# Kernel tuning notes

Measured on AMD Instinct MI355X. Metric: run time of the kernel, lower is better.

Reference implementation:

```python
import math
import jax, jax.numpy as jnp
import numpy as np

HEADS = 8
DIM_HEAD = 64
MAX_POS_EMB = 512


def setup_inputs() -> dict:
    key = jax.random.key(0)
    ks = jax.random.split(key, 6)
    dim = 512
    inner = HEADS * DIM_HEAD  # 512
    x = jax.random.normal(ks[0], (16, 3900, dim), jnp.float32)
    wq = jax.random.normal(ks[1], (dim, inner), jnp.float32) * 0.02
    wkv = jax.random.normal(ks[2], (dim, 2 * inner), jnp.float32) * 0.02
    wout_w = jax.random.normal(ks[3], (inner, dim), jnp.float32) * 0.02
    wout_b = jax.random.normal(ks[4], (dim,), jnp.float32) * 0.02
    rel_pos_table = jax.random.normal(ks[5], (2 * MAX_POS_EMB + 1, DIM_HEAD), jnp.float32) * 0.02
    return {"x": x, "wq": wq, "wkv": wkv, "wout_w": wout_w, "wout_b": wout_b,
            "rel_pos_table": rel_pos_table, "context_size": 200}


def reference(x, wq, wkv, wout_w, wout_b, rel_pos_table, context_size):
    bs, n, d = x.shape
    h, dh = HEADS, DIM_HEAD
    c = context_size
    scale = dh ** -0.5
    nb = math.ceil(n / c)
    nr = n % c
    if nr > 0:
        x = jnp.pad(x, ((0, 0), (0, c - nr), (0, 0)))  # [bs, nb*c, d]
    np_tok = nb * c
    q = x @ wq                     # [bs, np, inner]
    kv = x @ wkv                   # [bs, np, 2*inner]
    k, v = jnp.split(kv, 2, axis=-1)
    # [bs, nb, c, h, dh] -> [bs, nb, h, c, dh]
    def to_heads(t):
        return t.reshape(bs, nb, c, h, dh).transpose(0, 1, 3, 2, 4)
    q, k, v = to_heads(q), to_heads(k), to_heads(v)
    dots = jnp.einsum('bmhid,bmhjd->bmhij', q, k) * scale  # [bs, nb, h, c, c]
    # relative position bias (Transformer-XL style within chunk)
    seq = jnp.arange(c)
    dist = jnp.clip(seq[:, None] - seq[None, :], -c, c) + MAX_POS_EMB  # [c, c]
    rel = rel_pos_table[dist]  # [c, c, dh]
    pos_attn = jnp.einsum('bmhcd,crd->bmhcr', q, rel) * scale
    dots = dots + pos_attn
    if nr > 0:
        # last chunk: mask everything except the valid top-left nr x nr block
        mask = jnp.ones((c, c), dtype=bool).at[:nr, :nr].set(False)
        mask_value = -jnp.finfo(dots.dtype).max
        dots = dots.at[:, -1].set(jnp.where(mask, mask_value, dots[:, -1]))
    attn = jax.nn.softmax(dots, axis=-1)
    out = jnp.einsum('bmhij,bmhjd->bmhid', attn, v)  # [bs, nb, h, c, dh]
    out = out.transpose(0, 1, 3, 2, 4).reshape(bs, np_tok, h * dh)
    out = out[:, :n, :] @ wout_w + wout_b  # dropout is identity at eval
    return out
```

## Files before the change

### kernel.cpp

```cpp
#include <hip/hip_runtime.h>
#include <hip/hip_bf16.h>
#include <cstdint>
#include <cstddef>

#define BS 16
#define SEQ 3900
#define DIM 512
#define NHEAD 8
#define DH 64
#define CHUNK 200
#define NB 20
#define NR 100
#define NP 4000
#define MAXPOS 512
#define MD 62400

typedef __attribute__((ext_vector_type(8))) short bf16x8;
typedef __attribute__((ext_vector_type(8))) unsigned short u16x8;
typedef __attribute__((ext_vector_type(4))) float f32x4;
#define MFMA_BF16 __builtin_amdgcn_mfma_f32_16x16x32_bf16

static __device__ __forceinline__ float bf2f(unsigned short u) {
  union { unsigned int i; float f; } v; v.i = ((unsigned int)u) << 16; return v.f;
}
static __device__ __forceinline__ unsigned short f2bf(float f) {
  unsigned int x = __float_as_uint(f);
  unsigned int lsb = (x >> 16) & 1u;
  x += 0x7fffu + lsb;
  return (unsigned short)(x >> 16);
}

static __device__ __forceinline__ void gload16(const void* g, void* l) {
  auto gp = reinterpret_cast<const __attribute__((address_space(1))) unsigned int*>(
      reinterpret_cast<uintptr_t>(g));
  auto lp = reinterpret_cast<__attribute__((address_space(3))) unsigned int*>(
      reinterpret_cast<uintptr_t>(l));
  __builtin_amdgcn_global_load_lds(gp, lp, 16, 0, 0);
}

static __device__ __forceinline__ const unsigned short* wt_row(
    const unsigned short* base, int n) {
  unsigned ch = (unsigned)n / 100u;
  unsigned rr = (unsigned)n - ch * 100u;
  return base + (size_t)ch * (NP * DIM) + (size_t)SEQ * DIM + (size_t)rr * DIM;
}

__global__ __launch_bounds__(256) void prep_table(
    const float* __restrict__ table, unsigned short* __restrict__ Tb)
{
  int idx = (blockIdx.x * 256 + threadIdx.x) * 4;
  if (idx < 416 * 64) {
    float4 f = *reinterpret_cast<const float4*>(table + (size_t)305 * 64 + idx);
    ushort4 o;
    o.x = f2bf(f.x); o.y = f2bf(f.y); o.z = f2bf(f.z); o.w = f2bf(f.w);
    *reinterpret_cast<ushort4*>(Tb + idx) = o;
  }
}

__global__ __launch_bounds__(256) void wtrans(
    const float* __restrict__ W, int ldn, int n_off, float scale,
    unsigned short* __restrict__ base)
{
  __shared__ float ts[64][65];
  const int tid = threadIdx.x;
  const int n0 = blockIdx.x * 64;
  const int k0 = blockIdx.y * 64;
  {
    int kl = tid >> 4;
    int nl = (tid & 15) * 4;
#pragma unroll
    for (int p = 0; p < 4; ++p) {
      float4 f = *reinterpret_cast<const float4*>(
          W + (size_t)(k0 + kl + p * 16) * ldn + n0 + nl);
      ts[kl + p * 16][nl + 0] = f.x;
      ts[kl + p * 16][nl + 1] = f.y;
      ts[kl + p * 16][nl + 2] = f.z;
      ts[kl + p * 16][nl + 3] = f.w;
    }
  }
  __syncthreads();
  {
    int nl = tid >> 2;
    int kof = (tid & 3) * 16;
    int n = n0 + nl + n_off;
    unsigned ch = (unsigned)n / 100u;
    unsigned rr = (unsigned)n - ch * 100u;
    unsigned short* dst = base + (size_t)ch * (NP * DIM) + (size_t)SEQ * DIM
                          + (size_t)rr * DIM + k0 + kof;
    u16x8 o0, o1;
#pragma unroll
    for (int i = 0; i < 8; ++i) o0[i] = f2bf(ts[kof + i][nl] * scale);
#pragma unroll
    for (int i = 0; i < 8; ++i) o1[i] = f2bf(ts[kof + 8 + i][nl] * scale);
    *reinterpret_cast<u16x8*>(dst) = o0;
    *reinterpret_cast<u16x8*>(dst + 8) = o1;
  }
}

__global__ __launch_bounds__(256) void cast_x(
    const float* __restrict__ x, unsigned short* __restrict__ xb)
{
  const size_t total = (size_t)MD * DIM;
  size_t i = ((size_t)blockIdx.x * 256 + threadIdx.x) * 8;
  const size_t stride = (size_t)gridDim.x * 256 * 8;
  for (; i < total; i += stride) {
    float4 f0 = *reinterpret_cast<const float4*>(x + i);
    float4 f1 = *reinterpret_cast<const float4*>(x + i + 4);
    u16x8 o;
    o[0] = f2bf(f0.x); o[1] = f2bf(f0.y); o[2] = f2bf(f0.z); o[3] = f2bf(f0.w);
    o[4] = f2bf(f1.x); o[5] = f2bf(f1.y); o[6] = f2bf(f1.z); o[7] = f2bf(f1.w);
    *reinterpret_cast<u16x8*>(xb + i) = o;
  }
}

__global__ __launch_bounds__(256) void gemm_qkv(
    const unsigned short* __restrict__ xb, const unsigned short* __restrict__ WtBase,
    unsigned short* __restrict__ Qb, unsigned short* __restrict__ Kb,
    unsigned short* __restrict__ Vb)
{
  __shared__ unsigned short LDS[4][8 * 512];

  int bid = blockIdx.x;
  bid = (bid & 7) * 732 + (bid >> 3);
  const int bm = bid / 12, bn = bid % 12;
  const int m0 = bm * 128, n0 = bn * 128;
  const int tid = threadIdx.x;
  const int wv = tid >> 6, ln = tid & 63;
  const int wr = wv >> 1, wc = wv & 1;
  const int lr = ln & 15, lg = ln >> 4;

  const int sl = ln & 15, sk = (ln >> 4) * 8;
  const int q0 = wv * 2, q1 = q0 + 1;
  int ar0 = m0 + (q0 >> 2) * 64 + (q0 & 3) * 16 + sl; if (ar0 >= MD) ar0 = MD - 1;
  int ar1 = m0 + (q1 >> 2) * 64 + (q1 & 3) * 16 + sl; if (ar1 >= MD) ar1 = MD - 1;
  const unsigned short* aS0 = xb + (size_t)ar0 * DIM + sk;
  const unsigned short* aS1 = xb + (size_t)ar1 * DIM + sk;
  const unsigned short* bS0 = wt_row(WtBase, n0 + (q0 >> 2) * 64 + (q0 & 3) * 16 + sl) + sk;
  const unsigned short* bS1 = wt_row(WtBase, n0 + (q1 >> 2) * 64 + (q1 & 3) * 16 + sl) + sk;

  f32x4 acc[4][4];
#pragma unroll
  for (int i = 0; i < 4; ++i)
#pragma unroll
    for (int j = 0; j < 4; ++j) acc[i][j] = (f32x4){0.f, 0.f, 0.f, 0.f};

#define STG_QKV(buf, koff)                            \
  gload16(aS0 + (koff), &LDS[buf][q0 * 512]);         \
  gload16(aS1 + (koff), &LDS[buf][q1 * 512]);         \
  gload16(bS0 + (koff), &LDS[2 + buf][q0 * 512]);     \
  gload16(bS1 + (koff), &LDS[2 + buf][q1 * 512]);

  STG_QKV(0, 0)
  __syncthreads();

  int p = 0;
  for (int s = 0; s < 16; ++s) {
    if (s < 15) { STG_QKV(p ^ 1, (s + 1) * 32) }
    const unsigned short* asp = LDS[p];
    const unsigned short* bsp = LDS[2 + p];
    bf16x8 af[4], bfr[4];
#pragma unroll
    for (int mt = 0; mt < 4; ++mt)
      af[mt] = *reinterpret_cast<const bf16x8*>(asp + (wr * 4 + mt) * 512 + ln * 8);
#pragma unroll
    for (int nt = 0; nt < 4; ++nt)
      bfr[nt] = *reinterpret_cast<const bf16x8*>(bsp + (wc * 4 + nt) * 512 + ln * 8);
#pragma unroll
    for (int mt = 0; mt < 4; ++mt)
#pragma unroll
      for (int nt = 0; nt < 4; ++nt)
        acc[mt][nt] = MFMA_BF16(af[mt], bfr[nt], acc[mt][nt], 0, 0, 0);
    __syncthreads();
    p ^= 1;
  }

  unsigned short* dst; int nbase;
  if (n0 < 512)       { dst = Qb; nbase = 0; }
  else if (n0 < 1024) { dst = Kb; nbase = 512; }
  else                { dst = Vb; nbase = 1024; }
  const int dcol0 = n0 - nbase;

  unsigned char* Cb8 = reinterpret_cast<unsigned char*>(&LDS[0][0]);
#pragma unroll
  for (int mt = 0; mt < 4; ++mt) {
#pragma unroll
    for (int e = 0; e < 4; ++e) {
      int r = wr * 64 + mt * 16 + lg * 4 + e;
#pragma unroll
      for (int nt = 0; nt < 4; ++nt) {
        int c2 = (wc * 128 + nt * 32 + lr * 2) ^ (lg << 5);
        *reinterpret_cast<unsigned short*>(Cb8 + r * 256 + c2) = f2bf(acc[mt][nt][e]);
      }
    }
  }
  __syncthreads();
  {
    const int g = tid >> 4, l16 = tid & 15;
#pragma unroll
    for (int i = 0; i < 8; ++i) {
      int r = g * 8 + i;
      int off = (l16 * 16) ^ (((r >> 2) & 3) << 5);
      uint4 v = *reinterpret_cast<const uint4*>(Cb8 + r * 256 + off);
      unsigned rd = m0 + r;
      if (rd < MD) {
        unsigned bb = rd / 3900u;
        unsigned tt = rd - bb * 3900u;
        *reinterpret_cast<uint4*>(dst + ((size_t)bb * NP + tt) * DIM + dcol0 + l16 * 8) = v;
      }
    }
  }
}

__global__ __launch_bounds__(256) void gemm_out(
    const unsigned short* __restrict__ Ob, const unsigned short* __restrict__ WoBase,
    const float* __restrict__ bias, float* __restrict__ out)
{
  __shared__ unsigned short LDS[4][8 * 512];

  int bid = blockIdx.x;
  bid = (bid & 7) * 244 + (bid >> 3);
  const int bm = bid / 4, bn = bid % 4;
  const int m0 = bm * 128, n0 = bn * 128;
  const int tid = threadIdx.x;
  const int wv = tid >> 6, ln = tid & 63;
  const int wr = wv >> 1, wc = wv & 1;
  const int lr = ln & 15, lg = ln >> 4;

  const int sl = ln & 15, sk = (ln >> 4) * 8;
  const int q0 = wv * 2, q1 = q0 + 1;
  unsigned ar0 = m0 + (q0 >> 2) * 64 + (q0 & 3) * 16 + sl; if (ar0 >= MD) ar0 = MD - 1;
  unsigned ar1 = m0 + (q1 >> 2) * 64 + (q1 & 3) * 16 + sl; if (ar1 >= MD) ar1 = MD - 1;
  unsigned b0b = ar0 / 3900u, t0 = ar0 - b0b * 3900u;
  unsigned b1b = ar1 / 3900u, t1 = ar1 - b1b * 3900u;
  const unsigned short* aS0 = Ob + ((size_t)b0b * NP + t0) * DIM + sk;
  const unsigned short* aS1 = Ob + ((size_t)b1b * NP + t1) * DIM + sk;
  const unsigned short* bS0 = wt_row(WoBase, n0 + (q0 >> 2) * 64 + (q0 & 3) * 16 + sl) + sk;
  const unsigned short* bS1 = wt_row(WoBase, n0 + (q1 >> 2) * 64 + (q1 & 3) * 16 + sl) + sk;

  f32x4 acc[4][4];
#pragma unroll
  for (int i = 0; i < 4; ++i)
#pragma unroll
    for (int j = 0; j < 4; ++j) acc[i][j] = (f32x4){0.f, 0.f, 0.f, 0.f};

#define STG_OUT(buf, koff)                            \
  gload16(aS0 + (koff), &LDS[buf][q0 * 512]);         \
  gload16(aS1 + (koff), &LDS[buf][q1 * 512]);         \
  gload16(bS0 + (koff), &LDS[2 + buf][q0 * 512]);     \
  gload16(bS1 + (koff), &LDS[2 + buf][q1 * 512]);

  STG_OUT(0, 0)
  __syncthreads();

  int p = 0;
  for (int s = 0; s < 16; ++s) {
    if (s < 15) { STG_OUT(p ^ 1, (s + 1) * 32) }
    const unsigned short* asp = LDS[p];
    const unsigned short* bsp = LDS[2 + p];
    bf16x8 af[4], bfr[4];
#pragma unroll
    for (int mt = 0; mt < 4; ++mt)
      af[mt] = *reinterpret_cast<const bf16x8*>(asp + (wr * 4 + mt) * 512 + ln * 8);
#pragma unroll
    for (int nt = 0; nt < 4; ++nt)
      bfr[nt] = *reinterpret_cast<const bf16x8*>(bsp + (wc * 4 + nt) * 512 + ln * 8);
#pragma unroll
    for (int mt = 0; mt < 4; ++mt)
#pragma unroll
      for (int nt = 0; nt < 4; ++nt)
        acc[mt][nt] = MFMA_BF16(af[mt], bfr[nt], acc[mt][nt], 0, 0, 0);
    __syncthreads();
    p ^= 1;
  }

  char* Cf = reinterpret_cast<char*>(&LDS[0][0]);
  const int gg = tid >> 5, l32 = tid & 31;
#pragma unroll
  for (int pass = 0; pass < 2; ++pass) {
    if (wr == pass) {
#pragma unroll
      for (int mt = 0; mt < 4; ++mt)
#pragma unroll
        for (int e = 0; e < 4; ++e) {
          int rl = mt * 16 + lg * 4 + e;
#pragma unroll
          for (int nt = 0; nt < 4; ++nt) {
            int c4 = (wc * 256 + nt * 64 + lr * 4) ^ (lg << 6);
            *reinterpret_cast<float*>(Cf + rl * 512 + c4) = acc[mt][nt][e];
          }
        }
    }
    __syncthreads();
#pragma unroll
    for (int i = 0; i < 8; ++i) {
      int rl = gg * 8 + i;
      int off = (l32 * 16) ^ (((rl >> 2) & 3) << 6);
      float4 v = *reinterpret_cast<const float4*>(Cf + rl * 512 + off);
      int c = l32 * 4;
      float4 bv4 = *reinterpret_cast<const float4*>(bias + n0 + c);
      v.x += bv4.x; v.y += bv4.y; v.z += bv4.z; v.w += bv4.w;
      unsigned rd = m0 + pass * 64 + rl;
      if (rd < MD)
        *reinterpret_cast<float4*>(out + (size_t)rd * DIM + n0 + c) = v;
    }
    if (pass == 0) __syncthreads();
  }
}

#define KS_U16 12800
#define VT_U16 13568
#define PQ_STR 228
#define PQ_U16 (16*PQ_STR)
#define ATTN_LDS_B ((KS_U16 + VT_U16 + 4*PQ_U16) * 2)

__global__ __launch_bounds__(256) void attn_mfma(
    const unsigned short* __restrict__ Qb, const unsigned short* __restrict__ Kb,
    const unsigned short* __restrict__ Vb, const unsigned short* __restrict__ Tb,
    unsigned short* __restrict__ Ob)
{
  extern __shared__ unsigned short smem[];
  unsigned short* Ks = smem;
  unsigned short* Vt = smem + KS_U16;

  const int tid = threadIdx.x;
  const int bid = blockIdx.x;
  const int h  = bid & 7;
  const int bm = bid >> 3;
  const int m  = bm % NB;
  const int b  = bm / NB;
  const size_t rowbase = (size_t)b * NP + (size_t)m * CHUNK;
  const int lim = (m == NB - 1) ? NR : CHUNK;

  for (int c = tid; c < CHUNK * 8; c += 256) {
    int j = c >> 3, k0 = (c & 7) * 8;
    uint4 kv = *reinterpret_cast<const uint4*>(Kb + (rowbase + j) * DIM + h * DH + k0);
    int byte = (j * 128 + k0 * 2) ^ ((j & 7) << 4);
    *reinterpret_cast<uint4*>(reinterpret_cast<char*>(Ks) + byte) = kv;
    uint4 vv4 = *reinterpret_cast<const uint4*>(Vb + (rowbase + j) * DIM + h * DH + k0);
    const unsigned short* vs = reinterpret_cast<const unsigned short*>(&vv4);
#pragma unroll
    for (int e = 0; e < 8; ++e)
      Vt[(k0 + e) * 212 + j] = vs[e];
  }
  __syncthreads();

  const int wv = tid >> 6, ln = tid & 63;
  const int lr = ln & 15, lg = ln >> 4;
  unsigned short* pq = smem + KS_U16 + VT_U16 + wv * PQ_U16;

  const int nMt = (lim + 15) >> 4;
  for (int mt = wv; mt < nMt; mt += 4) {
    const int i0 = mt << 4;

    const unsigned short* qp = Qb + (rowbase + i0 + lr) * DIM + h * DH + lg * 8;
    bf16x8 qa0 = *reinterpret_cast<const bf16x8*>(qp);
    bf16x8 qa1 = *reinterpret_cast<const bf16x8*>(qp + 32);

#pragma unroll
    for (int ct = 0; ct < 14; ++ct) {
      const unsigned short* tp = Tb + (size_t)(i0 + ct * 16 + lr) * 64 + lg * 8;
      bf16x8 tb0 = *reinterpret_cast<const bf16x8*>(tp);
      bf16x8 tb1 = *reinterpret_cast<const bf16x8*>(tp + 32);
      f32x4 acc = {0.f, 0.f, 0.f, 0.f};
      acc = MFMA_BF16(qa0, tb0, acc, 0, 0, 0);
      acc = MFMA_BF16(qa1, tb1, acc, 0, 0, 0);
#pragma unroll
      for (int e = 0; e < 4; ++e)
        pq[(lg * 4 + e) * PQ_STR + ct * 16 + lr] = f2bf(acc[e]);
    }

    f32x4 s[13];
#pragma unroll
    for (int nt = 0; nt < 13; ++nt) {
      int row = nt * 16 + lr;
      int b0 = (row * 128 + lg * 16) ^ ((row & 7) << 4);
      int b1 = (row * 128 + 64 + lg * 16) ^ ((row & 7) << 4);
      bf16x8 k0 = *reinterpret_cast<const bf16x8*>(reinterpret_cast<char*>(Ks) + b0);
      bf16x8 k1 = *reinterpret_cast<const bf16x8*>(reinterpret_cast<char*>(Ks) + b1);
      f32x4 acc = {0.f, 0.f, 0.f, 0.f};
      acc = MFMA_BF16(qa0, k0, acc, 0, 0, 0);
      acc = MFMA_BF16(qa1, k1, acc, 0, 0, 0);
      s[nt] = acc;
    }

    float sv[4] = {0.f, 0.f, 0.f, 0.f};
#pragma unroll
    for (int nt = 0; nt < 13; ++nt) {
      int j = nt * 16 + lr;
#pragma unroll
      for (int e = 0; e < 4; ++e) {
        int r = lg * 4 + e;
        float pos = bf2f(pq[r * PQ_STR + (r - j + 207)]);
        float t = s[nt][e] + pos;
        float p = (j < lim) ? exp2f(t) : 0.f;
        s[nt][e] = p;
        sv[e] += p;
      }
    }
#pragma unroll
    for (int e = 0; e < 4; ++e) {
      float x = sv[e];
      x += __shfl_xor(x, 1);
      x += __shfl_xor(x, 2);
      x += __shfl_xor(x, 4);
      x += __shfl_xor(x, 8);
      sv[e] = __builtin_amdgcn_rcpf(x);
    }

#pragma unroll
    for (int nt = 0; nt < 13; ++nt)
#pragma unroll
      for (int e = 0; e < 4; ++e)
        pq[(lg * 4 + e) * PQ_STR + nt * 16 + lr] = f2bf(s[nt][e]);

    f32x4 o[4];
#pragma unroll
    for (int nt = 0; nt < 4; ++nt) o[nt] = (f32x4){0.f, 0.f, 0.f, 0.f};
    const ushort4 zz = {0, 0, 0, 0};
#pragma unroll
    for (int ks = 0; ks < 7; ++ks) {
      union __align__(16) { struct { ushort4 lo, hi; } u; bf16x8 v; } pa;
      if (ks < 6 || lg < 2) {
        const char* pap = reinterpret_cast<const char*>(pq) + lr * (PQ_STR * 2) + ks * 64 + lg * 16;
        pa.u.lo = *reinterpret_cast<const ushort4*>(pap);
        pa.u.hi = *reinterpret_cast<const ushort4*>(pap + 8);
      } else {
        pa.u.lo = zz; pa.u.hi = zz;
      }
#pragma unroll
      for (int nt = 0; nt < 4; ++nt) {
        union __align__(16) { struct { ushort4 lo, hi; } u; bf16x8 v; } vb;
        if (ks < 6 || lg == 0) {
          const char* vbp = reinterpret_cast<const char*>(Vt) + (nt * 16 + lr) * 424 + ks * 64 + lg * 16;
          vb.u.lo = *reinterpret_cast<const ushort4*>(vbp);
          vb.u.hi = *reinterpret_cast<const ushort4*>(vbp + 8);
        } else {
          vb.u.lo = zz; vb.u.hi = zz;
        }
        o[nt] = MFMA_BF16(pa.v, vb.v, o[nt], 0, 0, 0);
      }
    }

#pragma unroll
    for (int nt = 0; nt < 4; ++nt)
#pragma unroll
      for (int e = 0; e < 4; ++e) {
        int i = i0 + lg * 4 + e;
        if (i < lim) {
          Ob[(rowbase + i) * DIM + h * DH + nt * 16 + lr] = f2bf(o[nt][e] * sv[e]);
        }
      }
  }
}

extern "C" void kernel_launch(void* const* d_in, const int* in_sizes, int n_in,
                              void* d_out, int out_size, void* d_ws, size_t ws_size,
                              hipStream_t stream) {
  const float* x   = (const float*)d_in[0];
  const float* wq  = (const float*)d_in[1];
  const float* wkv = (const float*)d_in[2];
  const float* wo  = (const float*)d_in[3];
  const float* wb  = (const float*)d_in[4];
  const float* tbl = (const float*)d_in[5];
  float* out = (float*)d_out;

  const size_t elems = (size_t)BS * NP * DIM;
  unsigned short* Qb = (unsigned short*)d_ws;
  unsigned short* Kb = Qb + elems;
  unsigned short* Vb = Kb + elems;
  unsigned short* Ob = Qb;
  unsigned short* Tb = Kb + (size_t)SEQ * DIM;
  unsigned short* xb = (unsigned short*)d_out;

  hipFuncSetAttribute(reinterpret_cast<const void*>(attn_mfma),
                      hipFuncAttributeMaxDynamicSharedMemorySize, ATTN_LDS_B);

  const float qscale = 0.125f * 1.44269504088896f;
  dim3 blk(256);
  prep_table<<<dim3(26), blk, 0, stream>>>(tbl, Tb);
  wtrans<<<dim3(8, 8),  blk, 0, stream>>>(wq,  512,  0,   qscale, Qb);
  wtrans<<<dim3(16, 8), blk, 0, stream>>>(wkv, 1024, 512, 1.0f,   Qb);
  wtrans<<<dim3(8, 8),  blk, 0, stream>>>(wo,  512,  0,   1.0f,   Vb);
  cast_x<<<dim3(2048), blk, 0, stream>>>(x, xb);
  gemm_qkv<<<dim3(5856), blk, 0, stream>>>(xb, Qb, Qb, Kb, Vb);
  attn_mfma<<<dim3(BS * NB * NHEAD), blk, ATTN_LDS_B, stream>>>(Qb, Kb, Vb, Tb, Ob);
  gemm_out<<<dim3(1952), blk, 0, stream>>>(Ob, Vb, wb, out);
}
```

Measured before the change: 501.8 us.

## Merge prep kernels into one launch and read K directly from global in attention

Folds the table conversion, the three weight-transpose launches and the x cast into a single prep_all kernel dispatched by block index, cutting four kernel launches. In the attention kernel, K is no longer staged in LDS; each lane loads its K fragments straight from global memory, shrinking LDS use, which may allow more resident blocks. The positional-score tile is also shifted by 8 rows, letting the V-transpose and pq strides narrow and the last column tile's stores be skipped. The risk is extra global/L2 traffic for K, which is reread by every wave.

Measured after the change: 823.9 us. +64.2%, slower.

```diff
diff --git a/kernel.cpp b/kernel.cpp
--- a/kernel.cpp
+++ b/kernel.cpp
@@ -45,26 +45,14 @@
   return base + (size_t)ch * (NP * DIM) + (size_t)SEQ * DIM + (size_t)rr * DIM;
 }
 
-__global__ __launch_bounds__(256) void prep_table(
-    const float* __restrict__ table, unsigned short* __restrict__ Tb)
-{
-  int idx = (blockIdx.x * 256 + threadIdx.x) * 4;
-  if (idx < 416 * 64) {
-    float4 f = *reinterpret_cast<const float4*>(table + (size_t)305 * 64 + idx);
-    ushort4 o;
-    o.x = f2bf(f.x); o.y = f2bf(f.y); o.z = f2bf(f.z); o.w = f2bf(f.w);
-    *reinterpret_cast<ushort4*>(Tb + idx) = o;
-  }
-}
-
-__global__ __launch_bounds__(256) void wtrans(
+static __device__ void wtrans_body(
     const float* __restrict__ W, int ldn, int n_off, float scale,
-    unsigned short* __restrict__ base)
+    unsigned short* __restrict__ base, int nb, int kb)
 {
   __shared__ float ts[64][65];
   const int tid = threadIdx.x;
-  const int n0 = blockIdx.x * 64;
-  const int k0 = blockIdx.y * 64;
+  const int n0 = nb * 64;
+  const int k0 = kb * 64;
   {
     int kl = tid >> 4;
     int nl = (tid & 15) * 4;
@@ -97,12 +85,38 @@
   }
 }
 
-__global__ __launch_bounds__(256) void cast_x(
-    const float* __restrict__ x, unsigned short* __restrict__ xb)
+#define CAST_BLOCKS 2048
+#define PREP_BLOCKS (64 + 128 + 64 + 26 + CAST_BLOCKS)
+
+__global__ __launch_bounds__(256) void prep_all(
+    const float* __restrict__ x, const float* __restrict__ wq,
+    const float* __restrict__ wkv, const float* __restrict__ wo,
+    const float* __restrict__ tbl,
+    unsigned short* __restrict__ Qb, unsigned short* __restrict__ Vb,
+    unsigned short* __restrict__ Tb, unsigned short* __restrict__ xb,
+    float qscale)
 {
+  int bid = blockIdx.x;
+  if (bid < 64) { wtrans_body(wq, 512, 0, qscale, Qb, bid & 7, bid >> 3); return; }
+  bid -= 64;
+  if (bid < 128) { wtrans_body(wkv, 1024, 512, 1.0f, Qb, bid & 15, bid >> 4); return; }
+  bid -= 128;
+  if (bid < 64) { wtrans_body(wo, 512, 0, 1.0f, Vb, bid & 7, bid >> 3); return; }
+  bid -= 64;
+  if (bid < 26) {
+    int idx = (bid * 256 + threadIdx.x) * 4;
+    if (idx < 416 * 64) {
+      float4 f = *reinterpret_cast<const float4*>(tbl + (size_t)305 * 64 + idx);
+      ushort4 o;
+      o.x = f2bf(f.x); o.y = f2bf(f.y); o.z = f2bf(f.z); o.w = f2bf(f.w);
+      *reinterpret_cast<ushort4*>(Tb + idx) = o;
+    }
+    return;
+  }
+  bid -= 26;
   const size_t total = (size_t)MD * DIM;
-  size_t i = ((size_t)blockIdx.x * 256 + threadIdx.x) * 8;
-  const size_t stride = (size_t)gridDim.x * 256 * 8;
+  size_t i = ((size_t)bid * 256 + threadIdx.x) * 8;
+  const size_t stride = (size_t)CAST_BLOCKS * 256 * 8;
   for (; i < total; i += stride) {
     float4 f0 = *reinterpret_cast<const float4*>(x + i);
     float4 f1 = *reinterpret_cast<const float4*>(x + i + 4);
@@ -307,11 +321,10 @@
   }
 }
 
-#define KS_U16 12800
-#define VT_U16 13568
-#define PQ_STR 228
+#define VT_U16 (64*210)
+#define PQ_STR 216
 #define PQ_U16 (16*PQ_STR)
-#define ATTN_LDS_B ((KS_U16 + VT_U16 + 4*PQ_U16) * 2)
+#define ATTN_LDS_B ((VT_U16 + 4*PQ_U16) * 2)
 
 __global__ __launch_bounds__(256) void attn_mfma(
     const unsigned short* __restrict__ Qb, const unsigned short* __restrict__ Kb,
@@ -319,8 +332,7 @@
     unsigned short* __restrict__ Ob)
 {
   extern __shared__ unsigned short smem[];
-  unsigned short* Ks = smem;
-  unsigned short* Vt = smem + KS_U16;
+  unsigned short* Vt = smem;
 
   const int tid = threadIdx.x;
   const int bid = blockIdx.x;
@@ -333,20 +345,17 @@
 
   for (int c = tid; c < CHUNK * 8; c += 256) {
     int j = c >> 3, k0 = (c & 7) * 8;
-    uint4 kv = *reinterpret_cast<const uint4*>(Kb + (rowbase + j) * DIM + h * DH + k0);
-    int byte = (j * 128 + k0 * 2) ^ ((j & 7) << 4);
-    *reinterpret_cast<uint4*>(reinterpret_cast<char*>(Ks) + byte) = kv;
     uint4 vv4 = *reinterpret_cast<const uint4*>(Vb + (rowbase + j) * DIM + h * DH + k0);
     const unsigned short* vs = reinterpret_cast<const unsigned short*>(&vv4);
 #pragma unroll
     for (int e = 0; e < 8; ++e)
-      Vt[(k0 + e) * 212 + j] = vs[e];
+      Vt[(k0 + e) * 210 + j] = vs[e];
   }
   __syncthreads();
 
   const int wv = tid >> 6, ln = tid & 63;
   const int lr = ln & 15, lg = ln >> 4;
-  unsigned short* pq = smem + KS_U16 + VT_U16 + wv * PQ_U16;
+  unsigned short* pq = smem + VT_U16 + wv * PQ_U16;
 
   const int nMt = (lim + 15) >> 4;
   for (int mt = wv; mt < nMt; mt += 4) {
@@ -358,25 +367,26 @@
 
 #pragma unroll
     for (int ct = 0; ct < 14; ++ct) {
-      const unsigned short* tp = Tb + (size_t)(i0 + ct * 16 + lr) * 64 + lg * 8;
+      const unsigned short* tp = Tb + (size_t)(i0 + 8 + ct * 16 + lr) * 64 + lg * 8;
       bf16x8 tb0 = *reinterpret_cast<const bf16x8*>(tp);
       bf16x8 tb1 = *reinterpret_cast<const bf16x8*>(tp + 32);
       f32x4 acc = {0.f, 0.f, 0.f, 0.f};
       acc = MFMA_BF16(qa0, tb0, acc, 0, 0, 0);
       acc = MFMA_BF16(qa1, tb1, acc, 0, 0, 0);
-#pragma unroll
-      for (int e = 0; e < 4; ++e)
-        pq[(lg * 4 + e) * PQ_STR + ct * 16 + lr] = f2bf(acc[e]);
+      if (ct < 13 || lr < 7) {
+#pragma unroll
+        for (int e = 0; e < 4; ++e)
+          pq[(lg * 4 + e) * PQ_STR + ct * 16 + lr] = f2bf(acc[e]);
+      }
     }
 
     f32x4 s[13];
 #pragma unroll
     for (int nt = 0; nt < 13; ++nt) {
-      int row = nt * 16 + lr;
-      int b0 = (row * 128 + lg * 16) ^ ((row & 7) << 4);
-      int b1 = (row * 128 + 64 + lg * 16) ^ ((row & 7) << 4);
-      bf16x8 k0 = *reinterpret_cast<const bf16x8*>(reinterpret_cast<char*>(Ks) + b0);
-      bf16x8 k1 = *reinterpret_cast<const bf16x8*>(reinterpret_cast<char*>(Ks) + b1);
+      int kr = nt * 16 + lr; if (kr > CHUNK - 1) kr = CHUNK - 1;
+      const unsigned short* kp = Kb + (rowbase + kr) * DIM + h * DH + lg * 8;
+      bf16x8 k0 = *reinterpret_cast<const bf16x8*>(kp);
+      bf16x8 k1 = *reinterpret_cast<const bf16x8*>(kp + 32);
       f32x4 acc = {0.f, 0.f, 0.f, 0.f};
       acc = MFMA_BF16(qa0, k0, acc, 0, 0, 0);
       acc = MFMA_BF16(qa1, k1, acc, 0, 0, 0);
@@ -390,7 +400,7 @@
 #pragma unroll
       for (int e = 0; e < 4; ++e) {
         int r = lg * 4 + e;
-        float pos = bf2f(pq[r * PQ_STR + (r - j + 207)]);
+        float pos = bf2f(pq[r * PQ_STR + (r - j + 199)]);
         float t = s[nt][e] + pos;
         float p = (j < lim) ? exp2f(t) : 0.f;
         s[nt][e] = p;
@@ -431,7 +441,7 @@
       for (int nt = 0; nt < 4; ++nt) {
         union __align__(16) { struct { ushort4 lo, hi; } u; bf16x8 v; } vb;
         if (ks < 6 || lg == 0) {
-          const char* vbp = reinterpret_cast<const char*>(Vt) + (nt * 16 + lr) * 424 + ks * 64 + lg * 16;
+          const char* vbp = reinterpret_cast<const char*>(Vt) + (nt * 16 + lr) * 420 + ks * 64 + lg * 16;
           vb.u.lo = *reinterpret_cast<const ushort4*>(vbp);
           vb.u.hi = *reinterpret_cast<const ushort4*>(vbp + 8);
         } else {
@@ -476,13 +486,9 @@
                       hipFuncAttributeMaxDynamicSharedMemorySize, ATTN_LDS_B);
 
   const float qscale = 0.125f * 1.44269504088896f;
-  dim3 blk(256);
-  prep_table<<<dim3(26), blk, 0, stream>>>(tbl, Tb);
-  wtrans<<<dim3(8, 8),  blk, 0, stream>>>(wq,  512,  0,   qscale, Qb);
-  wtrans<<<dim3(16, 8), blk, 0, stream>>>(wkv, 1024, 512, 1.0f,   Qb);
-  wtrans<<<dim3(8, 8),  blk, 0, stream>>>(wo,  512,  0,   1.0f,   Vb);
-  cast_x<<<dim3(2048), blk, 0, stream>>>(x, xb);
-  gemm_qkv<<<dim3(5856), blk, 0, stream>>>(xb, Qb, Qb, Kb, Vb);
-  attn_mfma<<<dim3(BS * NB * NHEAD), blk, ATTN_LDS_B, stream>>>(Qb, Kb, Vb, Tb, Ob);
-  gemm_out<<<dim3(1952), blk, 0, stream>>>(Ob, Vb, wb, out);
-}
+  prep_all<<<dim3(PREP_BLOCKS), dim3(256), 0, stream>>>(
+      x, wq, wkv, wo, tbl, Qb, Vb, Tb, xb, qscale);
+  gemm_qkv<<<dim3(5856), dim3(256), 0, stream>>>(xb, Qb, Qb, Kb, Vb);
+  attn_mfma<<<dim3(BS * NB * NHEAD), dim3(256), ATTN_LDS_B, stream>>>(Qb, Kb, Vb, Tb, Ob);
+  gemm_out<<<dim3(1952), dim3(256), 0, stream>>>(Ob, Vb, wb, out);
+}
```
